# Optimization experiments

Hardware: AMD Instinct MI355X
Metric: run time of the kernel (lower is better)

## Reference

```python
import jax, jax.numpy as jnp
import numpy as np
import math

B, S, D = 2, 2048, 1024
H, KV, HD = 16, 4, 64
G = H // KV          # kv groups
CAP = 50.0           # attention soft-cap
EPS = 1e-6           # RMSNorm eps


def _rmsnorm(x, w):
    return x * jax.lax.rsqrt(jnp.mean(x * x, axis=-1, keepdims=True) + EPS) * w


def _rope(x, freqs):
    # x: (b, h, s, hd); freqs: (S, hd//2, 2) with [...,0]=cos, [...,1]=sin
    s = x.shape[2]
    xp = x.reshape(*x.shape[:-1], -1, 2)
    cos = freqs[:s, :, 0][None, None]   # (1,1,s,hd//2)
    sin = freqs[:s, :, 1][None, None]
    x0, x1 = xp[..., 0], xp[..., 1]
    out = jnp.stack([x0 * cos - x1 * sin, x0 * sin + x1 * cos], axis=-1)
    return out.reshape(x.shape)


def setup_inputs() -> dict:
    key = jax.random.key(0)
    ks = jax.random.split(key, 6)
    x = jax.random.normal(ks[0], (B, S, D), dtype=jnp.float32)
    # realistic RoPE table: theta_i = pos / 10000^(2i/hd)
    inv_freq = 1.0 / (10000.0 ** (np.arange(0, HD, 2, dtype=np.float32) / HD))
    theta = np.arange(S, dtype=np.float32)[:, None] * inv_freq[None, :]
    rope_freqs = jnp.asarray(np.stack([np.cos(theta), np.sin(theta)], axis=-1))
    sc = 0.02
    wq = jax.random.normal(ks[1], (2 * H * HD, D), dtype=jnp.float32) * sc
    wk = jax.random.normal(ks[2], (2 * KV * HD, D), dtype=jnp.float32) * sc
    wv = jax.random.normal(ks[3], (KV * HD, D), dtype=jnp.float32) * sc
    wo = jax.random.normal(ks[4], (D, H * HD), dtype=jnp.float32) * sc
    q_norm_w = jnp.ones((HD,), dtype=jnp.float32)
    k_norm_w = jnp.ones((HD,), dtype=jnp.float32)
    diff_lambda = jnp.array([0.8], dtype=jnp.float32)
    return {"x": x, "rope_freqs": rope_freqs, "wq": wq, "wk": wk, "wv": wv,
            "wo": wo, "q_norm_w": q_norm_w, "k_norm_w": k_norm_w,
            "diff_lambda": diff_lambda}


def reference(x, rope_freqs, wq, wk, wv, wo, q_norm_w, k_norm_w, diff_lambda):
    b, s, _ = x.shape
    # projections (torch Linear: y = x @ W^T)
    q = (x @ wq.T).reshape(b, s, H, 2 * HD).transpose(0, 2, 1, 3)   # (b,H,s,2hd)
    k = (x @ wk.T).reshape(b, s, KV, 2 * HD).transpose(0, 2, 1, 3)  # (b,KV,s,2hd)
    v = (x @ wv.T).reshape(b, s, KV, HD).transpose(0, 2, 1, 3)      # (b,KV,s,hd)
    q1, q2 = jnp.split(q, 2, axis=-1)
    k1, k2 = jnp.split(k, 2, axis=-1)
    # QK-norm (before RoPE, as in the torch module)
    q1, q2 = _rmsnorm(q1, q_norm_w), _rmsnorm(q2, q_norm_w)
    k1, k2 = _rmsnorm(k1, k_norm_w), _rmsnorm(k2, k_norm_w)
    # RoPE
    q1, q2 = _rope(q1, rope_freqs), _rope(q2, rope_freqs)
    k1, k2 = _rope(k1, rope_freqs), _rope(k2, rope_freqs)
    # GQA expansion: each kv head repeated G times contiguously
    k1 = jnp.repeat(k1, G, axis=1)
    k2 = jnp.repeat(k2, G, axis=1)
    v = jnp.repeat(v, G, axis=1)
    scale = 1.0 / math.sqrt(HD)
    scores1 = jnp.einsum('bhqd,bhkd->bhqk', q1, k1) * scale
    scores2 = jnp.einsum('bhqd,bhkd->bhqk', q2, k2) * scale
    # soft-cap
    scores1 = CAP * jnp.tanh(scores1 / CAP)
    scores2 = CAP * jnp.tanh(scores2 / CAP)
    mask = jnp.triu(jnp.full((s, s), -jnp.inf, dtype=scores1.dtype), 1)
    attn1 = jax.nn.softmax(scores1 + mask, axis=-1)
    attn2 = jax.nn.softmax(scores2 + mask, axis=-1)
    diff_attn = attn1 - diff_lambda[0] * attn2
    out = jnp.einsum('bhqk,bhkd->bhqd', diff_attn, v)
    out = out.transpose(0, 2, 1, 3).reshape(b, s, H * HD)
    return out @ wo.T
```

## Files before the change

kernel.cpp:

```cpp
#include <hip/hip_runtime.h>
#include <hip/hip_bf16.h>

#define B_ 2
#define S_ 2048
#define D_ 1024
#define H_ 16
#define KV_ 4
#define HD_ 64
#define G_ (H_ / KV_)
#define NCAT 2816
#define VOFF 2560

typedef __attribute__((ext_vector_type(8))) short short8;
typedef __attribute__((ext_vector_type(4))) short short4v;
typedef __attribute__((ext_vector_type(2))) int int2v;
typedef __attribute__((ext_vector_type(4))) int int4v;
typedef __attribute__((ext_vector_type(4))) float floatx4;

using gvoid_p = const __attribute__((address_space(1))) void*;
using lvoid_p = __attribute__((address_space(3))) void*;

__device__ inline void gload_lds16(const short* g, short* l) {
    __builtin_amdgcn_global_load_lds((gvoid_p)(const void*)g, (lvoid_p)(void*)l, 16, 0, 0);
}

__device__ inline int cvt_pk_bf16(float lo, float hi) {
    int r;
    asm volatile("v_cvt_pk_bf16_f32 %0, %1, %2" : "=v"(r) : "v"(lo), "v"(hi));
    return r;
}

__device__ inline float bf16lo(unsigned u) {
    return __builtin_bit_cast(float, u << 16);
}
__device__ inline float bf16hi(unsigned u) {
    return __builtin_bit_cast(float, u & 0xffff0000u);
}

__global__ void cvt5_kernel(const float* s0, const float* s1, const float* s2,
                            const float* s3, const float* s4,
                            __hip_bfloat16* d0, __hip_bfloat16* d1, __hip_bfloat16* d2,
                            __hip_bfloat16* d3, __hip_bfloat16* d4,
                            int n0, int n1, int n2, int n3, int n4) {
    const float* s; __hip_bfloat16* d; int n;
    switch (blockIdx.y) {
        case 0: s = s0; d = d0; n = n0; break;
        case 1: s = s1; d = d1; n = n1; break;
        case 2: s = s2; d = d2; n = n2; break;
        case 3: s = s3; d = d3; n = n3; break;
        default: s = s4; d = d4; n = n4; break;
    }
    int nv = n >> 2;
    for (int i = blockIdx.x * blockDim.x + threadIdx.x; i < nv;
         i += gridDim.x * blockDim.x) {
        floatx4 v = ((const floatx4*)s)[i];
        short4v o;
#pragma unroll
        for (int e = 0; e < 4; ++e) {
            __hip_bfloat16 hh = __float2bfloat16(v[e]);
            o[e] = __builtin_bit_cast(short, hh);
        }
        ((short4v*)d)[i] = o;
    }
}

__global__ __launch_bounds__(256) void gemm_qkv_fused(const short* __restrict__ A,
                                                      const short* __restrict__ Bm,
                                                      __hip_bfloat16* __restrict__ qout,
                                                      __hip_bfloat16* __restrict__ kout,
                                                      __hip_bfloat16* __restrict__ vout,
                                                      const float* __restrict__ freqs,
                                                      const float* __restrict__ qnw,
                                                      const float* __restrict__ knw,
                                                      int M, int N, int K) {
    __shared__ __align__(16) short As[2][128 * 32];
    __shared__ __align__(16) short Bs[2][128 * 32];
    int tid = threadIdx.x;
    int wid = tid >> 6, lane = tid & 63;
    int wr = wid >> 1, wc = wid & 1;
    int r = lane & 15, kq = lane >> 4;

    int nwg = gridDim.x * gridDim.y;
    int orig = blockIdx.y * gridDim.x + blockIdx.x;
    int wg = (orig & 7) * (nwg >> 3) + (orig >> 3);
    int bx = wg % gridDim.x, by = wg / gridDim.x;

    long m0 = (long)by * 128;
    long n0 = (long)bx * 128;

    const short* gA0 = A + (m0 + (tid >> 2)) * (long)K + (tid & 3) * 8;
    const short* gA1 = A + (m0 + 64 + (tid >> 2)) * (long)K + (tid & 3) * 8;
    const short* gB0 = Bm + (n0 + (tid >> 2)) * (long)K + (tid & 3) * 8;
    const short* gB1 = Bm + (n0 + 64 + (tid >> 2)) * (long)K + (tid & 3) * 8;

    auto stage = [&](int buf, int k0) {
        gload_lds16(gA0 + k0, &As[buf][wid * 512]);
        gload_lds16(gA1 + k0, &As[buf][2048 + wid * 512]);
        gload_lds16(gB0 + k0, &Bs[buf][wid * 512]);
        gload_lds16(gB1 + k0, &Bs[buf][2048 + wid * 512]);
    };

    floatx4 acc[4][4];
#pragma unroll
    for (int i = 0; i < 4; ++i)
#pragma unroll
        for (int j = 0; j < 4; ++j) acc[i][j] = {0.f, 0.f, 0.f, 0.f};

    int nt = K >> 5;
    stage(0, 0);
    for (int t = 0; t < nt; ++t) {
        int cur = t & 1;
        __builtin_amdgcn_s_barrier();
        if (t + 1 < nt) {
            stage(cur ^ 1, (t + 1) << 5);
            asm volatile("s_waitcnt vmcnt(4)" ::: "memory");
        } else {
            asm volatile("s_waitcnt vmcnt(0)" ::: "memory");
        }
        __builtin_amdgcn_sched_barrier(0);
        __builtin_amdgcn_s_barrier();
        short8 a[4], b[4];
#pragma unroll
        for (int mi = 0; mi < 4; ++mi)
            a[mi] = *(const short8*)&As[cur][(wr * 64 + mi * 16 + r) * 32 + kq * 8];
#pragma unroll
        for (int ni = 0; ni < 4; ++ni)
            b[ni] = *(const short8*)&Bs[cur][(wc * 64 + ni * 16 + r) * 32 + kq * 8];
#pragma unroll
        for (int mi = 0; mi < 4; ++mi)
#pragma unroll
            for (int ni = 0; ni < 4; ++ni)
                acc[mi][ni] = __builtin_amdgcn_mfma_f32_16x16x32_bf16(
                    a[mi], b[ni], acc[mi][ni], 0, 0, 0);
    }

    int col_l = lane & 15;
    int gbase = (int)n0 + wc * 64;
    int par = col_l & 1;
    if (gbase < VOFF) {
        const float* wnorm = (gbase < 2048) ? qnw : knw;
        float wv4[4];
        int fo[4];
#pragma unroll
        for (int ni = 0; ni < 4; ++ni) {
            wv4[ni] = wnorm[ni * 16 + col_l];
            fo[ni] = ni * 16 + (col_l >> 1) * 2;
        }
        __hip_bfloat16* outp;
        long tstride;
        int cbase;
        if (gbase < 2048) { outp = qout; tstride = 2048; cbase = gbase; }
        else              { outp = kout; tstride = 512;  cbase = gbase - 2048; }
#pragma unroll
        for (int mi = 0; mi < 4; ++mi) {
#pragma unroll
            for (int j = 0; j < 4; ++j) {
                int t = (int)m0 + wr * 64 + mi * 16 + kq * 4 + j;
                float ss = 0.f;
#pragma unroll
                for (int ni = 0; ni < 4; ++ni)
                    ss = fmaf(acc[mi][ni][j], acc[mi][ni][j], ss);
                ss += __shfl_xor(ss, 1); ss += __shfl_xor(ss, 2);
                ss += __shfl_xor(ss, 4); ss += __shfl_xor(ss, 8);
                float rr = rsqrtf(ss * (1.f / 64.f) + 1e-6f);
                const float* fb = freqs + (long)(t & (S_ - 1)) * 64;
                __hip_bfloat16* orow = outp + (long)t * tstride + cbase;
#pragma unroll
                for (int ni = 0; ni < 4; ++ni) {
                    float xv = acc[mi][ni][j] * rr * wv4[ni];
                    float pp = __shfl_xor(xv, 1);
                    float cc = fb[fo[ni]], sn = fb[fo[ni] + 1];
                    float y = par ? fmaf(pp, sn, xv * cc) : fmaf(xv, cc, -(pp * sn));
                    orow[ni * 16 + col_l] = __float2bfloat16(y);
                }
            }
        }
    } else {
        int kvv = (gbase - VOFF) >> 6;
#pragma unroll
        for (int mi = 0; mi < 4; ++mi) {
#pragma unroll
            for (int j = 0; j < 4; ++j) {
                int t = (int)m0 + wr * 64 + mi * 16 + kq * 4 + j;
                int bb = t >> 11, st = t & (S_ - 1);
                __hip_bfloat16* vcol = vout + ((long)(bb * KV_ + kvv) * 64) * S_ + st;
#pragma unroll
                for (int ni = 0; ni < 4; ++ni)
                    vcol[(long)(ni * 16 + col_l) * S_] = __float2bfloat16(acc[mi][ni][j]);
            }
        }
    }
}

template <typename OutT>
__global__ __launch_bounds__(256) void gemm_bt_lds(const short* __restrict__ A,
                                                   const short* __restrict__ Bm,
                                                   OutT* __restrict__ C,
                                                   int M, int N, int K) {
    __shared__ __align__(16) short As[2][128 * 32];
    __shared__ __align__(16) short Bs[2][128 * 32];
    int tid = threadIdx.x;
    int wid = tid >> 6, lane = tid & 63;
    int wr = wid >> 1, wc = wid & 1;
    int r = lane & 15, kq = lane >> 4;

    int nwg = gridDim.x * gridDim.y;
    int orig = blockIdx.y * gridDim.x + blockIdx.x;
    int wg = (orig & 7) * (nwg >> 3) + (orig >> 3);
    int bx = wg % gridDim.x, by = wg / gridDim.x;

    long m0 = (long)by * 128;
    long n0 = (long)bx * 128;

    const short* gA0 = A + (m0 + (tid >> 2)) * (long)K + (tid & 3) * 8;
    const short* gA1 = A + (m0 + 64 + (tid >> 2)) * (long)K + (tid & 3) * 8;
    const short* gB0 = Bm + (n0 + (tid >> 2)) * (long)K + (tid & 3) * 8;
    const short* gB1 = Bm + (n0 + 64 + (tid >> 2)) * (long)K + (tid & 3) * 8;

    auto stage = [&](int buf, int k0) {
        gload_lds16(gA0 + k0, &As[buf][wid * 512]);
        gload_lds16(gA1 + k0, &As[buf][2048 + wid * 512]);
        gload_lds16(gB0 + k0, &Bs[buf][wid * 512]);
        gload_lds16(gB1 + k0, &Bs[buf][2048 + wid * 512]);
    };

    floatx4 acc[4][4];
#pragma unroll
    for (int i = 0; i < 4; ++i)
#pragma unroll
        for (int j = 0; j < 4; ++j) acc[i][j] = {0.f, 0.f, 0.f, 0.f};

    int nt = K >> 5;
    stage(0, 0);
    for (int t = 0; t < nt; ++t) {
        int cur = t & 1;
        __builtin_amdgcn_s_barrier();
        if (t + 1 < nt) {
            stage(cur ^ 1, (t + 1) << 5);
            asm volatile("s_waitcnt vmcnt(4)" ::: "memory");
        } else {
            asm volatile("s_waitcnt vmcnt(0)" ::: "memory");
        }
        __builtin_amdgcn_sched_barrier(0);
        __builtin_amdgcn_s_barrier();
        short8 a[4], b[4];
#pragma unroll
        for (int mi = 0; mi < 4; ++mi)
            a[mi] = *(const short8*)&As[cur][(wr * 64 + mi * 16 + r) * 32 + kq * 8];
#pragma unroll
        for (int ni = 0; ni < 4; ++ni)
            b[ni] = *(const short8*)&Bs[cur][(wc * 64 + ni * 16 + r) * 32 + kq * 8];
#pragma unroll
        for (int mi = 0; mi < 4; ++mi)
#pragma unroll
            for (int ni = 0; ni < 4; ++ni)
                acc[mi][ni] = __builtin_amdgcn_mfma_f32_16x16x32_bf16(
                    a[mi], b[ni], acc[mi][ni], 0, 0, 0);
    }
    int col_l = lane & 15, row_l = (lane >> 4) * 4;
#pragma unroll
    for (int mi = 0; mi < 4; ++mi)
#pragma unroll
        for (int ni = 0; ni < 4; ++ni) {
            long col = n0 + wc * 64 + ni * 16 + col_l;
            long row0 = m0 + wr * 64 + mi * 16 + row_l;
#pragma unroll
            for (int j = 0; j < 4; ++j) {
                float v = acc[mi][ni][j];
                if constexpr (__is_same(OutT, float))
                    C[(row0 + j) * N + col] = v;
                else
                    C[(row0 + j) * N + col] = __float2bfloat16(v);
            }
        }
}

__global__ __launch_bounds__(512, 4) void attn_kernel(const short* __restrict__ qb,
                                                      const short* __restrict__ kbuf,
                                                      const short* __restrict__ vtb,
                                                      __hip_bfloat16* __restrict__ ob,
                                                      unsigned* __restrict__ part,
                                                      float* __restrict__ lpart,
                                                      const float* __restrict__ lam_p) {
    __shared__ __align__(16) short Ks[3][32][128];
    __shared__ __align__(16) short Vt[2][64][40];

    int tid = threadIdx.x, w = tid >> 6, lane = tid & 63;
    int raw = (int)blockIdx.x;
    int xcd = raw & 7;
    int kv = xcd & 3, b = xcd >> 2;
    int i5 = raw >> 3;
    int x = i5 & 15, hh = i5 >> 4;
    int h = kv * G_ + hh;
    int p = x >> 1, e = x & 1;
    int qtA = p, qtB = 15 - p;
    int r = lane & 15, kq = lane >> 4;
    bool w4 = (w < 4);
    float lam = lam_p[0];

    floatx4 acc[2][4];
    floatx4 accl[2];
    short8 qa[2][2];

    const short* vbase = vtb + (long)(b * KV_ + kv) * 64 * S_;
    const float c1 = 0.18033688f, nc4 = -3.7570e-7f, zoff = -17.3123405f;
    const short one_bf = (short)0x3F80;
    short8 ones8 = {one_bf, one_bf, one_bf, one_bf, one_bf, one_bf, one_bf, one_bf};

    int krow0 = tid >> 4, kcs0 = ((tid & 15) ^ (krow0 & 7)) * 8;
    const short* kgb = kbuf + ((long)b * S_ * KV_ + kv) * 128;
    int vd = (tid >> 2) & 63, vch = tid & 3;

    auto issueK = [&](int buf, int ki) {
        long rb = (long)(ki * 32) * (KV_ * 128);
        gload_lds16(kgb + rb + (long)krow0 * (KV_ * 128) + kcs0, &Ks[buf][0][0] + w * 512);
    };
    auto loadV = [&](int kb) {
        return *(const short8*)(vbase + (long)vd * S_ + kb + vch * 8);
    };

    auto reset_acc = [&]() {
#pragma unroll
        for (int m = 0; m < 2; ++m) {
            accl[m] = {0.f, 0.f, 0.f, 0.f};
#pragma unroll
            for (int dt = 0; dt < 4; ++dt) acc[m][dt] = {0.f, 0.f, 0.f, 0.f};
        }
    };
    auto load_q = [&](int q0) {
        const short* qrow = qb + ((long)(b * S_ + q0 + r) * H_ + h) * 128;
        qa[0][0] = *(const short8*)(qrow + kq * 8);
        qa[0][1] = *(const short8*)(qrow + 32 + kq * 8);
        qa[1][0] = *(const short8*)(qrow + 64 + kq * 8);
        qa[1][1] = *(const short8*)(qrow + 96 + kq * 8);
    };

    auto tile_compute = [&](int bk, int cv, int kb, int q0, bool domask) {
        int rel = q0 + r - kb;
        short8 vb[4];
#pragma unroll
        for (int dt = 0; dt < 4; ++dt) {
            const short* vrow = &Vt[cv][dt * 16 + r][0];
            int2v lo = *(const int2v*)(vrow + 4 * kq);
            int2v hi = *(const int2v*)(vrow + 16 + 4 * kq);
            vb[dt] = __builtin_bit_cast(short8, int4v{lo[0], lo[1], hi[0], hi[1]});
        }
#pragma unroll
        for (int m = 0; m < 2; ++m) {
            floatx4 sacc[2];
            __builtin_amdgcn_s_setprio(1);
#pragma unroll
            for (int nt = 0; nt < 2; ++nt) {
                sacc[nt] = {0.f, 0.f, 0.f, 0.f};
                const short* row = &Ks[bk][nt * 16 + r][0];
                short8 a0 = *(const short8*)(row + (((m * 8) + kq) ^ (r & 7)) * 8);
                short8 a1 = *(const short8*)(row + (((m * 8) + 4 + kq) ^ (r & 7)) * 8);
                sacc[nt] = __builtin_amdgcn_mfma_f32_16x16x32_bf16(a0, qa[m][0], sacc[nt], 0, 0, 0);
                sacc[nt] = __builtin_amdgcn_mfma_f32_16x16x32_bf16(a1, qa[m][1], sacc[nt], 0, 0, 0);
            }
            __builtin_amdgcn_s_setprio(0);
            float pv[2][4];
#pragma unroll
            for (int nt = 0; nt < 2; ++nt)
#pragma unroll
                for (int j = 0; j < 4; ++j) {
                    float rawv = sacc[nt][j];
                    float r2 = rawv * rawv;
                    float z = fmaf(rawv, fmaf(r2, nc4, c1), zoff);
                    pv[nt][j] = __builtin_amdgcn_exp2f(z);
                }
            if (domask) {
#pragma unroll
                for (int nt = 0; nt < 2; ++nt)
#pragma unroll
                    for (int j = 0; j < 4; ++j)
                        if (nt * 16 + kq * 4 + j > rel) pv[nt][j] = 0.f;
            }
            int d0 = cvt_pk_bf16(pv[0][0], pv[0][1]);
            int d1 = cvt_pk_bf16(pv[0][2], pv[0][3]);
            int d2 = cvt_pk_bf16(pv[1][0], pv[1][1]);
            int d3 = cvt_pk_bf16(pv[1][2], pv[1][3]);
            short8 pa8 = __builtin_bit_cast(short8, int4v{d0, d1, d2, d3});
            __builtin_amdgcn_s_setprio(1);
#pragma unroll
            for (int dt = 0; dt < 4; ++dt)
                acc[m][dt] = __builtin_amdgcn_mfma_f32_16x16x32_bf16(
                    pa8, vb[dt], acc[m][dt], 0, 0, 0);
            accl[m] = __builtin_amdgcn_mfma_f32_16x16x32_bf16(pa8, ones8, accl[m], 0, 0, 0);
            __builtin_amdgcn_s_setprio(0);
        }
    };

    auto run = [&](int qt, int ki0, int ki1, bool diag) {
        int q0 = qt * 128 + w * 16;
        load_q(q0);
        reset_acc();
        int nseg = ki1 - ki0;
        issueK(0, ki0);
        short8 rva = {}, rvb = {};
        if (w4) rva = loadV(ki0 * 32);
        int bk = 0;
        for (int ii = 0; ii < nseg; ++ii) {
            int ki = ki0 + ii, cv = ii & 1;
            bool pre = (ii + 1 < nseg);
            int bk1 = (bk == 2) ? 0 : bk + 1;
            if (pre) issueK(bk1, ki + 1);
            if (pre) asm volatile("s_waitcnt vmcnt(1)" ::: "memory");
            else     asm volatile("s_waitcnt vmcnt(0)" ::: "memory");
            __builtin_amdgcn_sched_barrier(0);
            if (cv == 0) {
                if (w4) {
                    *(short8*)&Vt[0][vd][vch * 8] = rva;
                    if (pre) rvb = loadV((ki + 1) * 32);
                }
            } else {
                if (w4) {
                    *(short8*)&Vt[1][vd][vch * 8] = rvb;
                    if (pre) rva = loadV((ki + 1) * 32);
                }
            }
            asm volatile("s_waitcnt lgkmcnt(0)" ::: "memory");
            __builtin_amdgcn_sched_barrier(0);
            __builtin_amdgcn_s_barrier();
            tile_compute(bk, cv, ki * 32, q0, diag && (ki >= 4 * qt));
            bk = bk1;
        }
        __builtin_amdgcn_s_barrier();
    };

    if (e == 0) {
        run(qtA, 0, 4 * qtA + 4, true);
        {
            int q0 = qtA * 128 + w * 16;
#pragma unroll
            for (int j = 0; j < 4; ++j) {
                float i1 = 1.f / accl[0][j];
                float i2 = lam / accl[1][j];
                int qr = q0 + kq * 4 + j;
                __hip_bfloat16* orow = ob + ((long)(b * S_ + qr) * H_ + h) * 64;
#pragma unroll
                for (int dt = 0; dt < 4; ++dt) {
                    float val = acc[0][dt][j] * i1 - acc[1][dt][j] * i2;
                    orow[dt * 16 + r] = __float2bfloat16(val);
                }
            }
        }
        run(qtB, 0, 30 - 4 * p, false);
    } else {
        run(qtB, 30 - 4 * p, 64 - 4 * p, true);
    }

    {
        long slot = (long)(b * H_ + h) * 8 + (qtB - 8);
        long base = (slot * 2 + e) * 8192L;
        int qloc = w * 16 + kq * 4;
#pragma unroll
        for (int dt = 0; dt < 4; ++dt)
#pragma unroll
            for (int j = 0; j < 4; ++j)
                part[base + (qloc + j) * 64 + dt * 16 + r] =
                    (unsigned)cvt_pk_bf16(acc[0][dt][j], acc[1][dt][j]);
        if (r == 0) {
#pragma unroll
            for (int m = 0; m < 2; ++m)
#pragma unroll
                for (int j = 0; j < 4; ++j)
                    lpart[((slot * 2 + e) * 2 + m) * 128 + qloc + j] = accl[m][j];
        }
    }
}

__global__ __launch_bounds__(256) void attn_merge_kernel(const unsigned* __restrict__ part,
                                                         const float* __restrict__ lpart,
                                                         __hip_bfloat16* __restrict__ ob,
                                                         const float* __restrict__ lam_p) {
    long sid = blockIdx.x;
    int t8 = sid & 7;
    int h = (sid >> 3) & (H_ - 1);
    int b = (int)(sid >> 7);
    int qt = 8 + t8;
    float lam = lam_p[0];
    const unsigned* p0 = part + sid * 2 * 8192L;
    const unsigned* p1 = p0 + 8192;
    const float* l0 = lpart + sid * 512L;
    const float* l1 = l0 + 256;
    int tid = threadIdx.x;
#pragma unroll
    for (int i = 0; i < 32; ++i) {
        int idx = i * 256 + tid;
        int q = idx >> 6, d = idx & 63;
        unsigned u0 = p0[q * 64 + d], u1 = p1[q * 64 + d];
        float a1 = bf16lo(u0) + bf16lo(u1);
        float a2 = bf16hi(u0) + bf16hi(u1);
        float L1 = l0[q] + l1[q];
        float L2 = l0[128 + q] + l1[128 + q];
        float val = a1 / L1 - lam * (a2 / L2);
        ob[((long)(b * S_ + qt * 128 + q) * H_ + h) * 64 + d] = __float2bfloat16(val);
    }
}

extern "C" void kernel_launch(void* const* d_in, const int* in_sizes, int n_in,
                              void* d_out, int out_size, void* d_ws, size_t ws_size,
                              hipStream_t stream) {
    const float* x     = (const float*)d_in[0];
    const float* freqs = (const float*)d_in[1];
    const float* wq    = (const float*)d_in[2];
    const float* wk    = (const float*)d_in[3];
    const float* wv    = (const float*)d_in[4];
    const float* wo    = (const float*)d_in[5];
    const float* qnw   = (const float*)d_in[6];
    const float* knw   = (const float*)d_in[7];
    const float* lam   = (const float*)d_in[8];
    float* out = (float*)d_out;

    const int T = B_ * S_;
    char* ws = (char*)d_ws;
    size_t off = 0;
    auto alloc = [&](size_t bytes) {
        void* p = ws + off;
        off += (bytes + 255) & ~(size_t)255;
        return p;
    };
    __hip_bfloat16* xb   = (__hip_bfloat16*)alloc((size_t)T * D_ * 2);
    __hip_bfloat16* wcat = (__hip_bfloat16*)alloc((size_t)NCAT * D_ * 2);
    __hip_bfloat16* wob  = (__hip_bfloat16*)alloc((size_t)D_ * D_ * 2);
    __hip_bfloat16* qb16 = (__hip_bfloat16*)alloc((size_t)T * 2 * H_ * HD_ * 2);
    __hip_bfloat16* kb16 = (__hip_bfloat16*)alloc((size_t)T * 2 * KV_ * HD_ * 2);
    __hip_bfloat16* vT   = (__hip_bfloat16*)alloc((size_t)B_ * KV_ * HD_ * S_ * 2);
    unsigned* part = (unsigned*)alloc((size_t)256 * 2 * 8192 * 4);
    float* lpart   = (float*)alloc((size_t)256 * 2 * 2 * 128 * 4);
    __hip_bfloat16* aob  = xb;

    cvt5_kernel<<<dim3(2048, 5), 256, 0, stream>>>(
        x, wq, wk, wv, wo,
        xb, wcat, wcat + (size_t)2 * H_ * HD_ * D_,
        wcat + (size_t)(2 * H_ * HD_ + 2 * KV_ * HD_) * D_, wob,
        T * D_, 2 * H_ * HD_ * D_, 2 * KV_ * HD_ * D_, KV_ * HD_ * D_, D_ * D_);

    gemm_qkv_fused<<<dim3(NCAT / 128, T / 128), 256, 0, stream>>>(
        (const short*)xb, (const short*)wcat, qb16, kb16, vT,
        freqs, qnw, knw, T, NCAT, D_);

    attn_kernel<<<512, 512, 0, stream>>>(
        (const short*)qb16, (const short*)kb16, (const short*)vT, aob, part, lpart, lam);
    attn_merge_kernel<<<256, 256, 0, stream>>>(part, lpart, aob, lam);

    gemm_bt_lds<float><<<dim3(D_ / 128, T / 128), 256, 0, stream>>>(
        (const short*)aob, (const short*)wob, out, T, D_, D_);
}
```

Baseline: 159.5 us.

## Process two K/V tiles per barrier with four-deep LDS buffering

Restructures the attention inner loop so each barrier covers two 32-key tiles instead of one. K and V buffers grow to four slots. Both wave halves now stage V, one tile each, and the next pair of K tiles is prefetched while the current pair is computed. The aim is to halve the number of barriers and waitcnt stalls per key range. In exchange it uses more LDS, which may lower occupancy at 4 blocks per CU, and it waits on vmcnt(0) before each pair, which reduces prefetch depth.

```diff
diff --git a/kernel.cpp b/kernel.cpp
--- a/kernel.cpp
+++ b/kernel.cpp
@@ -282,8 +282,8 @@
                                                       unsigned* __restrict__ part,
                                                       float* __restrict__ lpart,
                                                       const float* __restrict__ lam_p) {
-    __shared__ __align__(16) short Ks[3][32][128];
-    __shared__ __align__(16) short Vt[2][64][40];
+    __shared__ __align__(16) short Ks[4][32][128];
+    __shared__ __align__(16) short Vt[4][64][40];
 
     int tid = threadIdx.x, w = tid >> 6, lane = tid & 63;
     int raw = (int)blockIdx.x;
@@ -310,6 +310,7 @@
     int krow0 = tid >> 4, kcs0 = ((tid & 15) ^ (krow0 & 7)) * 8;
     const short* kgb = kbuf + ((long)b * S_ * KV_ + kv) * 128;
     int vd = (tid >> 2) & 63, vch = tid & 3;
+    int vsel = w4 ? 0 : 1;
 
     auto issueK = [&](int buf, int ki) {
         long rb = (long)(ki * 32) * (KV_ * 128);
@@ -397,33 +398,37 @@
         reset_acc();
         int nseg = ki1 - ki0;
         issueK(0, ki0);
-        short8 rva = {}, rvb = {};
-        if (w4) rva = loadV(ki0 * 32);
-        int bk = 0;
-        for (int ii = 0; ii < nseg; ++ii) {
-            int ki = ki0 + ii, cv = ii & 1;
-            bool pre = (ii + 1 < nseg);
-            int bk1 = (bk == 2) ? 0 : bk + 1;
-            if (pre) issueK(bk1, ki + 1);
-            if (pre) asm volatile("s_waitcnt vmcnt(1)" ::: "memory");
-            else     asm volatile("s_waitcnt vmcnt(0)" ::: "memory");
-            __builtin_amdgcn_sched_barrier(0);
-            if (cv == 0) {
-                if (w4) {
-                    *(short8*)&Vt[0][vd][vch * 8] = rva;
-                    if (pre) rvb = loadV((ki + 1) * 32);
-                }
-            } else {
-                if (w4) {
-                    *(short8*)&Vt[1][vd][vch * 8] = rvb;
-                    if (pre) rva = loadV((ki + 1) * 32);
-                }
-            }
+        if (nseg > 1) issueK(1, ki0 + 1);
+        short8 rva = {};
+        if (vsel < nseg) rva = loadV((ki0 + vsel) * 32);
+        int ii = 0;
+        for (; ii + 1 < nseg; ii += 2) {
+            int vb0 = 2 * ((ii >> 1) & 1);
+            *(short8*)&Vt[vb0 + vsel][vd][vch * 8] = rva;
+            asm volatile("s_waitcnt vmcnt(0)" ::: "memory");
             asm volatile("s_waitcnt lgkmcnt(0)" ::: "memory");
             __builtin_amdgcn_sched_barrier(0);
             __builtin_amdgcn_s_barrier();
-            tile_compute(bk, cv, ki * 32, q0, diag && (ki >= 4 * qt));
-            bk = bk1;
+            if (ii + 2 < nseg) {
+                issueK((ii + 2) & 3, ki0 + ii + 2);
+                if (ii + 3 < nseg) issueK((ii + 3) & 3, ki0 + ii + 3);
+                int nxt = ii + 2 + vsel;
+                if (nxt < nseg) rva = loadV((ki0 + nxt) * 32);
+            }
+            int ki = ki0 + ii;
+            tile_compute(ii & 3, vb0, ki * 32, q0, diag && (ki >= 4 * qt));
+            tile_compute((ii + 1) & 3, vb0 + 1, (ki + 1) * 32, q0,
+                         diag && (ki + 1 >= 4 * qt));
+        }
+        if (ii < nseg) {
+            int vb0 = 2 * ((ii >> 1) & 1);
+            if (w4) *(short8*)&Vt[vb0][vd][vch * 8] = rva;
+            asm volatile("s_waitcnt vmcnt(0)" ::: "memory");
+            asm volatile("s_waitcnt lgkmcnt(0)" ::: "memory");
+            __builtin_amdgcn_sched_barrier(0);
+            __builtin_amdgcn_s_barrier();
+            int ki = ki0 + ii;
+            tile_compute(ii & 3, vb0, ki * 32, q0, diag && (ki >= 4 * qt));
         }
         __builtin_amdgcn_s_barrier();
     };
```

Measured after the change: 156.6 us. No clear change (-1.8%).
